# Kernel optimization log

Measured on AMD Instinct MI355X. Metric: run time of the kernel, lower is better.

Reference implementation:

```python
import jax, jax.numpy as jnp
import numpy as np

B, N, C_IN, C_OUT = 8, 4096, 64, 64
NEG_INF = -9e15
LEAKY_SLOPE = 0.01  # torch F.leaky_relu default


def setup_inputs() -> dict:
    key = jax.random.key(0)
    kx, ka, kw, kq, kk = jax.random.split(key, 5)
    X = jax.random.normal(kx, (B, N, C_IN), dtype=jnp.float32)
    A = jax.random.randint(ka, (N, N), 0, 2, dtype=jnp.int32)
    # xavier_uniform with gain=1.414 ~ scaled uniform; plain scaled normal is fine for a numeric reference
    def xavier(k, shape):
        fan_in, fan_out = shape
        bound = 1.414 * np.sqrt(6.0 / (fan_in + fan_out))
        return jax.random.uniform(k, shape, jnp.float32, -bound, bound)
    weight = xavier(kw, (C_IN, C_OUT))
    query = xavier(kq, (C_IN, C_OUT))
    key_p = xavier(kk, (C_IN, C_OUT))
    return {"X": X, "A": A, "weight": weight, "query": query, "key_p": key_p}


def reference(X, A, weight, query, key_p):
    n = X.shape[1]
    idx = jnp.arange(n)
    adj = A.at[idx, idx].set(1)  # add self-loops
    out = jnp.einsum('bni,io->bno', X, weight)
    q = jnp.einsum('bni,io->bno', X, query)
    k = jnp.einsum('bni,io->bno', X, key_p)
    att = jnp.einsum('bnd,bmd->bnm', q, k)          # QK^T, (B,N,N)
    att = jax.nn.leaky_relu(att, LEAKY_SLOPE)
    att = jnp.where(adj[None, :, :] > 0, att, NEG_INF)
    att = jax.nn.softmax(att, axis=-1)
    # dropout p=0 and/or eval mode -> identity
    return jnp.einsum('bnm,bmo->bno', att, out)
```

## Files before the change

### kernel.cpp

```cpp
#include <hip/hip_runtime.h>
#include <stdint.h>

#define BATCH 8
#define NN 4096
#define CC 64
#define MASKV -1.0e30f
#define LOG2E 1.4426950408889634f

typedef _Float16 half8 __attribute__((ext_vector_type(8)));
typedef __fp16 fp16x2 __attribute__((ext_vector_type(2)));
typedef float f32x4 __attribute__((ext_vector_type(4)));

__global__ __launch_bounds__(256) void gat_proj(
    const float* __restrict__ X, const float* __restrict__ W0,
    const float* __restrict__ Wq, const float* __restrict__ Wk,
    _Float16* __restrict__ qh, _Float16* __restrict__ ql,
    _Float16* __restrict__ kb, _Float16* __restrict__ vt)
{
    __shared__ alignas(16) _Float16 WTh[3][64][72];
    __shared__ alignas(16) _Float16 WTl[3][64][72];
    const int t = threadIdx.x;
    const float* Ws[3] = {W0, Wq, Wk};
    for (int e = t; e < 4096; e += 256) {
        int k = e >> 6, c = e & 63;
        #pragma unroll
        for (int m = 0; m < 3; ++m) {
            float w = Ws[m][e];
            _Float16 hi = (_Float16)w;
            WTh[m][c][k] = hi;
            WTl[m][c][k] = (_Float16)(w - (float)hi);
        }
    }
    __syncthreads();
    const int lane = t & 63, wv = t >> 6;
    const int cl = lane & 15, g = lane >> 4;
    {
        int tile = blockIdx.x * 4 + wv;
        int gr = tile * 16;
        const float* xr = X + (size_t)(gr + cl) * CC;
        half8 xh[2], xl[2];
        #pragma unroll
        for (int kf = 0; kf < 2; ++kf) {
            f32x4 a0 = *(const f32x4*)(xr + g*8 + kf*32);
            f32x4 a1 = *(const f32x4*)(xr + g*8 + kf*32 + 4);
            half8 h, l;
            #pragma unroll
            for (int j = 0; j < 4; ++j) {
                _Float16 h0 = (_Float16)a0[j], h1 = (_Float16)a1[j];
                h[j]   = h0; l[j]   = (_Float16)(a0[j] - (float)h0);
                h[j+4] = h1; l[j+4] = (_Float16)(a1[j] - (float)h1);
            }
            xh[kf] = h; xl[kf] = l;
        }
        #pragma unroll
        for (int mat = 1; mat <= 2; ++mat) {
            #pragma unroll
            for (int nt = 0; nt < 4; ++nt) {
                f32x4 acc = {0.f, 0.f, 0.f, 0.f};
                #pragma unroll
                for (int kf = 0; kf < 2; ++kf) {
                    half8 bh = *(const half8*)&WTh[mat][nt*16 + cl][g*8 + kf*32];
                    half8 bl = *(const half8*)&WTl[mat][nt*16 + cl][g*8 + kf*32];
                    acc = __builtin_amdgcn_mfma_f32_16x16x32_f16(xh[kf], bh, acc, 0, 0, 0);
                    acc = __builtin_amdgcn_mfma_f32_16x16x32_f16(xl[kf], bh, acc, 0, 0, 0);
                    acc = __builtin_amdgcn_mfma_f32_16x16x32_f16(xh[kf], bl, acc, 0, 0, 0);
                }
                #pragma unroll
                for (int i = 0; i < 4; ++i) {
                    size_t off = (size_t)(gr + 4*g + i) * CC + nt*16 + cl;
                    if (mat == 1) {
                        float qs = acc[i] * LOG2E;
                        _Float16 hi = (_Float16)qs;
                        qh[off] = hi;
                        ql[off] = (_Float16)(qs - (float)hi);
                    } else {
                        kb[off] = (_Float16)acc[i];
                    }
                }
            }
        }
        {
            int b = gr >> 12, n0 = gr & (NN - 1);
            #pragma unroll
            for (int mt = 0; mt < 4; ++mt) {
                f32x4 acc = {0.f, 0.f, 0.f, 0.f};
                #pragma unroll
                for (int kf = 0; kf < 2; ++kf) {
                    half8 ah = *(const half8*)&WTh[0][mt*16 + cl][g*8 + kf*32];
                    half8 al = *(const half8*)&WTl[0][mt*16 + cl][g*8 + kf*32];
                    acc = __builtin_amdgcn_mfma_f32_16x16x32_f16(ah, xh[kf], acc, 0, 0, 0);
                    acc = __builtin_amdgcn_mfma_f32_16x16x32_f16(al, xh[kf], acc, 0, 0, 0);
                    acc = __builtin_amdgcn_mfma_f32_16x16x32_f16(ah, xl[kf], acc, 0, 0, 0);
                }
                #pragma unroll
                for (int i = 0; i < 4; ++i) {
                    int co = mt*16 + 4*g + i;
                    vt[((size_t)b * CC + co) * NN + n0 + cl] = (_Float16)acc[i];
                }
            }
        }
    }
}

__global__ __launch_bounds__(256) void gat_mask(const int* __restrict__ A,
                                                unsigned short* __restrict__ M16)
{
    const int row = blockIdx.x;
    const int w16 = threadIdx.x;
    const int4* ap = (const int4*)(A + (size_t)row * NN + w16 * 16);
    unsigned m = 0;
    #pragma unroll
    for (int j = 0; j < 4; ++j) {
        int4 a = ap[j];
        m |= (a.x != 0 ? 1u : 0u) << (4*j);
        m |= (a.y != 0 ? 1u : 0u) << (4*j + 1);
        m |= (a.z != 0 ? 1u : 0u) << (4*j + 2);
        m |= (a.w != 0 ? 1u : 0u) << (4*j + 3);
    }
    if (w16 == (row >> 4)) m |= 1u << (row & 15);
    M16[(size_t)row * 256 + w16] = (unsigned short)m;
}

__global__ __launch_bounds__(256) void gat_attn(
    const _Float16* __restrict__ qh, const _Float16* __restrict__ ql,
    const _Float16* __restrict__ kf16, const _Float16* __restrict__ vtb,
    const unsigned long long* __restrict__ M,
    _Float16* __restrict__ po, float2* __restrict__ pml)
{
    __shared__ alignas(16) _Float16 Kt[64][72];
    __shared__ alignas(16) _Float16 Vt[64][72];
    __shared__ alignas(16) _Float16 Ps[4][32][72];
    const int t = threadIdx.x;
    const int lane = t & 63, wv = t >> 6;
    const int cl = lane & 15, g = lane >> 4;
    const int blk = blockIdx.x;
    const int b  = blk & 7;
    const int sp = (blk >> 3) & 3;
    const int qb = blk >> 5;
    const int Q0 = qb * 128 + wv * 32;
    const int c0 = sp * 16;

    half8 qfh[2][2], qfl[2][2];
    #pragma unroll
    for (int qt = 0; qt < 2; ++qt) {
        const _Float16* qrh = qh + ((size_t)b * NN + Q0 + qt*16 + cl) * CC;
        const _Float16* qrl = ql + ((size_t)b * NN + Q0 + qt*16 + cl) * CC;
        qfh[qt][0] = *(const half8*)(qrh + g*8);
        qfh[qt][1] = *(const half8*)(qrh + g*8 + 32);
        qfl[qt][0] = *(const half8*)(qrl + g*8);
        qfl[qt][1] = *(const half8*)(qrl + g*8 + 32);
    }
    const _Float16* kg = kf16 + (size_t)b * NN * CC;
    const _Float16* vg = vtb + (size_t)b * CC * NN;

    f32x4 o[2][4] = {};
    float m_run[2] = {MASKV, MASKV}, l_run[2] = {0.f, 0.f};

    uint4 pk0, pk1, pv0, pv1;
    unsigned long long pmA, pmB;
    auto loadchunk = [&](int kc) {
        const uint4* ks = (const uint4*)(kg + (size_t)kc * 64 * CC);
        pk0 = ks[t];
        pk1 = ks[t + 256];
        const _Float16* vs = vg + kc * 64;
        pv0 = *(const uint4*)(vs + (size_t)(t >> 3) * NN + (t & 7) * 8);
        pv1 = *(const uint4*)(vs + (size_t)((t >> 3) + 32) * NN + (t & 7) * 8);
        pmA = M[(size_t)(Q0 + cl) * 64 + kc];
        pmB = M[(size_t)(Q0 + 16 + cl) * 64 + kc];
    };
    loadchunk(c0);

    for (int kc = 0; kc < 16; ++kc) {
        __syncthreads();
        *(uint4*)&Kt[t >> 3][(t & 7) * 8] = pk0;
        *(uint4*)&Kt[(t >> 3) + 32][(t & 7) * 8] = pk1;
        *(uint4*)&Vt[t >> 3][(t & 7) * 8] = pv0;
        *(uint4*)&Vt[(t >> 3) + 32][(t & 7) * 8] = pv1;
        const unsigned long long cmA = pmA, cmB = pmB;
        __syncthreads();
        if (kc < 15) loadchunk(c0 + kc + 1);

        f32x4 sc[2][4] = {};
        #pragma unroll
        for (int kt = 0; kt < 4; ++kt) {
            #pragma unroll
            for (int kf = 0; kf < 2; ++kf) {
                half8 ka = *(const half8*)&Kt[kt*16 + cl][g*8 + kf*32];
                sc[0][kt] = __builtin_amdgcn_mfma_f32_16x16x32_f16(ka, qfh[0][kf], sc[0][kt], 0, 0, 0);
                sc[0][kt] = __builtin_amdgcn_mfma_f32_16x16x32_f16(ka, qfl[0][kf], sc[0][kt], 0, 0, 0);
                sc[1][kt] = __builtin_amdgcn_mfma_f32_16x16x32_f16(ka, qfh[1][kf], sc[1][kt], 0, 0, 0);
                sc[1][kt] = __builtin_amdgcn_mfma_f32_16x16x32_f16(ka, qfl[1][kf], sc[1][kt], 0, 0, 0);
            }
        }

        #pragma unroll
        for (int qt = 0; qt < 2; ++qt) {
            const unsigned long long cm = qt ? cmB : cmA;
            const unsigned mwx = (unsigned)cm, mwy = (unsigned)(cm >> 32);
            float sv[16];
            float mx = MASKV;
            #pragma unroll
            for (int kt = 0; kt < 4; ++kt) {
                unsigned wmw = (kt < 2) ? mwx : mwy;
                #pragma unroll
                for (int i = 0; i < 4; ++i) {
                    float x = sc[qt][kt][i];
                    x = fmaxf(x, 0.01f * x);
                    int bit = ((kt & 1) * 16) + 4*g + i;
                    x = ((wmw >> bit) & 1u) ? x : MASKV;
                    sv[kt*4 + i] = x;
                    mx = fmaxf(mx, x);
                }
            }
            mx = fmaxf(mx, __shfl_xor(mx, 16));
            mx = fmaxf(mx, __shfl_xor(mx, 32));
            if (__any(mx > m_run[qt])) {
                float nm = fmaxf(m_run[qt], mx);
                float alpha = __builtin_amdgcn_exp2f(m_run[qt] - nm);
                m_run[qt] = nm;
                l_run[qt] *= alpha;
                #pragma unroll
                for (int ct = 0; ct < 4; ++ct) o[qt][ct] *= alpha;
            }
            float lsum = 0.f;
            float p[16];
            #pragma unroll
            for (int j = 0; j < 16; ++j) {
                p[j] = __builtin_amdgcn_exp2f(sv[j] - m_run[qt]);
                lsum += p[j];
            }
            l_run[qt] += lsum;
            #pragma unroll
            for (int kt = 0; kt < 4; ++kt) {
                union { fp16x2 h; unsigned u; } p0u, p1u;
                p0u.h = __builtin_amdgcn_cvt_pkrtz(p[kt*4+0], p[kt*4+1]);
                p1u.h = __builtin_amdgcn_cvt_pkrtz(p[kt*4+2], p[kt*4+3]);
                uint2 pw = {p0u.u, p1u.u};
                *(uint2*)&Ps[wv][qt*16 + cl][kt*16 + 4*g] = pw;
            }
        }
        __builtin_amdgcn_wave_barrier();

        half8 pf[2][2];
        #pragma unroll
        for (int qt = 0; qt < 2; ++qt) {
            pf[qt][0] = *(const half8*)&Ps[wv][qt*16 + cl][g*8];
            pf[qt][1] = *(const half8*)&Ps[wv][qt*16 + cl][g*8 + 32];
        }
        #pragma unroll
        for (int ct = 0; ct < 4; ++ct) {
            half8 vf0 = *(const half8*)&Vt[ct*16 + cl][g*8];
            half8 vf1 = *(const half8*)&Vt[ct*16 + cl][g*8 + 32];
            #pragma unroll
            for (int qt = 0; qt < 2; ++qt) {
                o[qt][ct] = __builtin_amdgcn_mfma_f32_16x16x32_f16(vf0, pf[qt][0], o[qt][ct], 0, 0, 0);
                o[qt][ct] = __builtin_amdgcn_mfma_f32_16x16x32_f16(vf1, pf[qt][1], o[qt][ct], 0, 0, 0);
            }
        }
    }

    #pragma unroll
    for (int qt = 0; qt < 2; ++qt) {
        float lt = l_run[qt];
        lt += __shfl_xor(lt, 16);
        lt += __shfl_xor(lt, 32);
        size_t base = (size_t)sp * (BATCH * NN) + (size_t)b * NN + Q0 + qt*16 + cl;
        _Float16* orow = po + base * 64;
        #pragma unroll
        for (int ct = 0; ct < 4; ++ct) {
            union { fp16x2 h; unsigned u; } o0u, o1u;
            o0u.h = __builtin_amdgcn_cvt_pkrtz(o[qt][ct][0], o[qt][ct][1]);
            o1u.h = __builtin_amdgcn_cvt_pkrtz(o[qt][ct][2], o[qt][ct][3]);
            uint2 ow = {o0u.u, o1u.u};
            *(uint2*)(orow + ct*16 + 4*g) = ow;
        }
        if (g == 0) pml[base] = make_float2(m_run[qt], lt);
    }
}

__global__ __launch_bounds__(256) void gat_comb(
    const _Float16* __restrict__ po, const float2* __restrict__ pml,
    float* __restrict__ out)
{
    int gid = blockIdx.x * 256 + threadIdx.x;
    int row = gid >> 2;
    int col = (gid & 3) * 16;
    float2 ml[4];
    float Mx = MASKV;
    #pragma unroll
    for (int s = 0; s < 4; ++s) {
        ml[s] = pml[s * (BATCH * NN) + row];
        Mx = fmaxf(Mx, ml[s].x);
    }
    float w[4], den = 0.f;
    #pragma unroll
    for (int s = 0; s < 4; ++s) {
        w[s] = __builtin_amdgcn_exp2f(ml[s].x - Mx);
        den += w[s] * ml[s].y;
    }
    float inv = 1.0f / den;
    float acc[16] = {};
    #pragma unroll
    for (int s = 0; s < 4; ++s) {
        const _Float16* p = po + ((size_t)s * (BATCH * NN) + row) * 64 + col;
        float a = w[s] * inv;
        half8 v0 = *(const half8*)(p);
        half8 v1 = *(const half8*)(p + 8);
        #pragma unroll
        for (int j = 0; j < 8; ++j) {
            acc[j]     += a * (float)v0[j];
            acc[j + 8] += a * (float)v1[j];
        }
    }
    float* op = out + (size_t)row * 64 + col;
    #pragma unroll
    for (int i = 0; i < 4; ++i) {
        f32x4 r = {acc[4*i], acc[4*i+1], acc[4*i+2], acc[4*i+3]};
        *(f32x4*)(op + i*4) = r;
    }
}

extern "C" void kernel_launch(void* const* d_in, const int* in_sizes, int n_in,
                              void* d_out, int out_size, void* d_ws, size_t ws_size,
                              hipStream_t stream) {
    const float* X  = (const float*)d_in[0];
    const int*   A  = (const int*)d_in[1];
    const float* W0 = (const float*)d_in[2];
    const float* Wq = (const float*)d_in[3];
    const float* Wk = (const float*)d_in[4];
    float* out = (float*)d_out;
    char* ws = (char*)d_ws;
    const size_t SZ = (size_t)BATCH * NN * CC * 2;
    _Float16* qh  = (_Float16*)(ws);
    _Float16* ql  = (_Float16*)(ws + SZ);
    _Float16* kbf = (_Float16*)(ws + 2*SZ);
    _Float16* vtb = (_Float16*)(ws + 3*SZ);
    char* Mbase = ws + 4*SZ;
    _Float16* po = (_Float16*)(Mbase + 2*1024*1024);
    float2* pml  = (float2*)(Mbase + 2*1024*1024 + 4*SZ);

    hipLaunchKernelGGL(gat_proj, dim3(512),  dim3(256), 0, stream, X, W0, Wq, Wk, qh, ql, kbf, vtb);
    hipLaunchKernelGGL(gat_mask, dim3(4096), dim3(256), 0, stream, A, (unsigned short*)Mbase);
    hipLaunchKernelGGL(gat_attn, dim3(1024), dim3(256), 0, stream, qh, ql, kbf, vtb,
                       (const unsigned long long*)Mbase, po, pml);
    hipLaunchKernelGGL(gat_comb, dim3(512),  dim3(256), 0, stream, po, pml, out);
}
```

Before: 207.9 us.

## Use byte-mask adjacency, packed fp16 masking, XOR-swizzled LDS and MFMA priority

The mask kernel now writes a per-thread byte mask (16 MiB) laid out to match each lane's MFMA accumulator positions. The attention kernel applies the mask with packed fp16 bit operations and packed max, and zeroes masked probabilities by ANDing the mask. LDS tiles drop their padding in favour of an XOR swizzle. MFMA sections run at raised wave priority. The aim is fewer per-element shift/select ALU ops in the softmax and fewer LDS bank conflicts, at the cost of eight times more mask memory traffic and fp16 precision in the max and row-sum accumulation.

After: 209.6 us. Within noise of the previous version (+0.8%).

```diff
diff --git a/kernel.cpp b/kernel.cpp
--- a/kernel.cpp
+++ b/kernel.cpp
@@ -103,33 +103,35 @@
 }
 
 __global__ __launch_bounds__(256) void gat_mask(const int* __restrict__ A,
-                                                unsigned short* __restrict__ M16)
+                                                uint4* __restrict__ AM)
 {
-    const int row = blockIdx.x;
-    const int w16 = threadIdx.x;
-    const int4* ap = (const int4*)(A + (size_t)row * NN + w16 * 16);
-    unsigned m = 0;
-    #pragma unroll
-    for (int j = 0; j < 4; ++j) {
-        int4 a = ap[j];
-        m |= (a.x != 0 ? 1u : 0u) << (4*j);
-        m |= (a.y != 0 ? 1u : 0u) << (4*j + 1);
-        m |= (a.z != 0 ? 1u : 0u) << (4*j + 2);
-        m |= (a.w != 0 ? 1u : 0u) << (4*j + 3);
-    }
-    if (w16 == (row >> 4)) m |= 1u << (row & 15);
-    M16[(size_t)row * 256 + w16] = (unsigned short)m;
+    const int r = blockIdx.x;
+    const int t = threadIdx.x;
+    const int kc = t >> 2, g = t & 3;
+    unsigned w[4];
+    #pragma unroll
+    for (int kt = 0; kt < 4; ++kt) {
+        const int k0 = kc*64 + kt*16 + 4*g;
+        int4 a = *(const int4*)(A + (size_t)r * NN + k0);
+        unsigned m = 0;
+        m |= (a.x != 0 || k0     == r) ? 0x000000FFu : 0u;
+        m |= (a.y != 0 || k0 + 1 == r) ? 0x0000FF00u : 0u;
+        m |= (a.z != 0 || k0 + 2 == r) ? 0x00FF0000u : 0u;
+        m |= (a.w != 0 || k0 + 3 == r) ? 0xFF000000u : 0u;
+        w[kt] = m;
+    }
+    AM[(size_t)r * 256 + t] = make_uint4(w[0], w[1], w[2], w[3]);
 }
 
 __global__ __launch_bounds__(256) void gat_attn(
     const _Float16* __restrict__ qh, const _Float16* __restrict__ ql,
     const _Float16* __restrict__ kf16, const _Float16* __restrict__ vtb,
-    const unsigned long long* __restrict__ M,
+    const uint4* __restrict__ AM,
     _Float16* __restrict__ po, float2* __restrict__ pml)
 {
-    __shared__ alignas(16) _Float16 Kt[64][72];
-    __shared__ alignas(16) _Float16 Vt[64][72];
-    __shared__ alignas(16) _Float16 Ps[4][32][72];
+    __shared__ alignas(16) _Float16 Kt[64][64];
+    __shared__ alignas(16) _Float16 Vt[64][64];
+    __shared__ alignas(16) _Float16 Ps[4][32][64];
     const int t = threadIdx.x;
     const int lane = t & 63, wv = t >> 6;
     const int cl = lane & 15, g = lane >> 4;
@@ -139,6 +141,14 @@
     const int qb = blk >> 5;
     const int Q0 = qb * 128 + wv * 32;
     const int c0 = sp * 16;
+    const int swz = (cl & 7) << 4;
+
+    const int soff = (((t >> 3) * 128 + (t & 7) * 16) ^ (((t >> 3) & 7) << 4));
+    char* const kd0 = (char*)Kt + soff;
+    char* const kd1 = (char*)Kt + soff + 32 * 128;
+    char* const vd0 = (char*)Vt + soff;
+    char* const vd1 = (char*)Vt + soff + 32 * 128;
+    char* const psb = (char*)&Ps[wv][0][0];
 
     half8 qfh[2][2], qfl[2][2];
     #pragma unroll
@@ -156,8 +166,7 @@
     f32x4 o[2][4] = {};
     float m_run[2] = {MASKV, MASKV}, l_run[2] = {0.f, 0.f};
 
-    uint4 pk0, pk1, pv0, pv1;
-    unsigned long long pmA, pmB;
+    uint4 pk0, pk1, pv0, pv1, pa, pb;
     auto loadchunk = [&](int kc) {
         const uint4* ks = (const uint4*)(kg + (size_t)kc * 64 * CC);
         pk0 = ks[t];
@@ -165,53 +174,74 @@
         const _Float16* vs = vg + kc * 64;
         pv0 = *(const uint4*)(vs + (size_t)(t >> 3) * NN + (t & 7) * 8);
         pv1 = *(const uint4*)(vs + (size_t)((t >> 3) + 32) * NN + (t & 7) * 8);
-        pmA = M[(size_t)(Q0 + cl) * 64 + kc];
-        pmB = M[(size_t)(Q0 + 16 + cl) * 64 + kc];
+        pa = AM[(size_t)(Q0 + cl)      * 256 + kc * 4 + g];
+        pb = AM[(size_t)(Q0 + 16 + cl) * 256 + kc * 4 + g];
     };
     loadchunk(c0);
 
+    auto pkmax = [](unsigned a, unsigned b) {
+        unsigned d;
+        asm("v_pk_max_f16 %0, %1, %2" : "=v"(d) : "v"(a), "v"(b));
+        return d;
+    };
+
     for (int kc = 0; kc < 16; ++kc) {
         __syncthreads();
-        *(uint4*)&Kt[t >> 3][(t & 7) * 8] = pk0;
-        *(uint4*)&Kt[(t >> 3) + 32][(t & 7) * 8] = pk1;
-        *(uint4*)&Vt[t >> 3][(t & 7) * 8] = pv0;
-        *(uint4*)&Vt[(t >> 3) + 32][(t & 7) * 8] = pv1;
-        const unsigned long long cmA = pmA, cmB = pmB;
+        *(uint4*)kd0 = pk0;
+        *(uint4*)kd1 = pk1;
+        *(uint4*)vd0 = pv0;
+        *(uint4*)vd1 = pv1;
+        const uint4 ca = pa, cb = pb;
         __syncthreads();
         if (kc < 15) loadchunk(c0 + kc + 1);
 
+        __builtin_amdgcn_s_setprio(1);
         f32x4 sc[2][4] = {};
         #pragma unroll
         for (int kt = 0; kt < 4; ++kt) {
             #pragma unroll
             for (int kf = 0; kf < 2; ++kf) {
-                half8 ka = *(const half8*)&Kt[kt*16 + cl][g*8 + kf*32];
+                half8 ka = *(const half8*)((char*)Kt +
+                    ((((kt*16 + cl) * 128) + g*16 + kf*64) ^ swz));
                 sc[0][kt] = __builtin_amdgcn_mfma_f32_16x16x32_f16(ka, qfh[0][kf], sc[0][kt], 0, 0, 0);
                 sc[0][kt] = __builtin_amdgcn_mfma_f32_16x16x32_f16(ka, qfl[0][kf], sc[0][kt], 0, 0, 0);
                 sc[1][kt] = __builtin_amdgcn_mfma_f32_16x16x32_f16(ka, qfh[1][kf], sc[1][kt], 0, 0, 0);
                 sc[1][kt] = __builtin_amdgcn_mfma_f32_16x16x32_f16(ka, qfl[1][kf], sc[1][kt], 0, 0, 0);
             }
         }
+        __builtin_amdgcn_s_setprio(0);
 
         #pragma unroll
         for (int qt = 0; qt < 2; ++qt) {
-            const unsigned long long cm = qt ? cmB : cmA;
-            const unsigned mwx = (unsigned)cm, mwy = (unsigned)(cm >> 32);
+            const uint4 wm = qt ? cb : ca;
+            const unsigned am[4] = {wm.x, wm.y, wm.z, wm.w};
+            unsigned hm[8];
+            #pragma unroll
+            for (int kt = 0; kt < 4; ++kt) {
+                hm[2*kt]   = __builtin_amdgcn_perm(0u, am[kt], 0x01010000u);
+                hm[2*kt+1] = __builtin_amdgcn_perm(0u, am[kt], 0x03030202u);
+            }
             float sv[16];
-            float mx = MASKV;
+            #pragma unroll
+            for (int j = 0; j < 16; ++j) {
+                float x = sc[qt][j >> 2][j & 3];
+                sv[j] = fmaxf(x, 0.01f * x);
+            }
+            union UH { unsigned u; fp16x2 h; };
+            unsigned sm[8];
             #pragma unroll
             for (int kt = 0; kt < 4; ++kt) {
-                unsigned wmw = (kt < 2) ? mwx : mwy;
-                #pragma unroll
-                for (int i = 0; i < 4; ++i) {
-                    float x = sc[qt][kt][i];
-                    x = fmaxf(x, 0.01f * x);
-                    int bit = ((kt & 1) * 16) + 4*g + i;
-                    x = ((wmw >> bit) & 1u) ? x : MASKV;
-                    sv[kt*4 + i] = x;
-                    mx = fmaxf(mx, x);
-                }
-            }
+                UH s0, s1;
+                s0.h = __builtin_amdgcn_cvt_pkrtz(sv[4*kt + 0], sv[4*kt + 1]);
+                s1.h = __builtin_amdgcn_cvt_pkrtz(sv[4*kt + 2], sv[4*kt + 3]);
+                sm[2*kt]   = (hm[2*kt]   & s0.u) | (~hm[2*kt]   & 0xFC00FC00u);
+                sm[2*kt+1] = (hm[2*kt+1] & s1.u) | (~hm[2*kt+1] & 0xFC00FC00u);
+            }
+            unsigned tm = pkmax(
+                pkmax(pkmax(sm[0], sm[1]), pkmax(sm[2], sm[3])),
+                pkmax(pkmax(sm[4], sm[5]), pkmax(sm[6], sm[7])));
+            UH tmu; tmu.u = tm;
+            float mx = fmaxf((float)tmu.h[0], (float)tmu.h[1]);
             mx = fmaxf(mx, __shfl_xor(mx, 16));
             mx = fmaxf(mx, __shfl_xor(mx, 32));
             if (__any(mx > m_run[qt])) {
@@ -222,41 +252,45 @@
                 #pragma unroll
                 for (int ct = 0; ct < 4; ++ct) o[qt][ct] *= alpha;
             }
-            float lsum = 0.f;
             float p[16];
             #pragma unroll
-            for (int j = 0; j < 16; ++j) {
+            for (int j = 0; j < 16; ++j)
                 p[j] = __builtin_amdgcn_exp2f(sv[j] - m_run[qt]);
-                lsum += p[j];
-            }
-            l_run[qt] += lsum;
+            UH zz; zz.u = 0u;
+            fp16x2 acc2 = zz.h;
             #pragma unroll
             for (int kt = 0; kt < 4; ++kt) {
-                union { fp16x2 h; unsigned u; } p0u, p1u;
-                p0u.h = __builtin_amdgcn_cvt_pkrtz(p[kt*4+0], p[kt*4+1]);
-                p1u.h = __builtin_amdgcn_cvt_pkrtz(p[kt*4+2], p[kt*4+3]);
-                uint2 pw = {p0u.u, p1u.u};
-                *(uint2*)&Ps[wv][qt*16 + cl][kt*16 + 4*g] = pw;
-            }
+                UH w0, w1;
+                w0.h = __builtin_amdgcn_cvt_pkrtz(p[kt*4 + 0], p[kt*4 + 1]);
+                w1.h = __builtin_amdgcn_cvt_pkrtz(p[kt*4 + 2], p[kt*4 + 3]);
+                w0.u &= hm[2*kt];
+                w1.u &= hm[2*kt+1];
+                uint2 pw = {w0.u, w1.u};
+                *(uint2*)(psb + ((((qt*16 + cl) * 128) + kt*32 + g*8) ^ swz)) = pw;
+                acc2 += w0.h + w1.h;
+            }
+            l_run[qt] += (float)acc2[0] + (float)acc2[1];
         }
         __builtin_amdgcn_wave_barrier();
 
         half8 pf[2][2];
         #pragma unroll
         for (int qt = 0; qt < 2; ++qt) {
-            pf[qt][0] = *(const half8*)&Ps[wv][qt*16 + cl][g*8];
-            pf[qt][1] = *(const half8*)&Ps[wv][qt*16 + cl][g*8 + 32];
-        }
+            pf[qt][0] = *(const half8*)(psb + ((((qt*16 + cl) * 128) + g*16) ^ swz));
+            pf[qt][1] = *(const half8*)(psb + ((((qt*16 + cl) * 128) + g*16 + 64) ^ swz));
+        }
+        __builtin_amdgcn_s_setprio(1);
         #pragma unroll
         for (int ct = 0; ct < 4; ++ct) {
-            half8 vf0 = *(const half8*)&Vt[ct*16 + cl][g*8];
-            half8 vf1 = *(const half8*)&Vt[ct*16 + cl][g*8 + 32];
+            half8 vf0 = *(const half8*)((char*)Vt + ((((ct*16 + cl) * 128) + g*16) ^ swz));
+            half8 vf1 = *(const half8*)((char*)Vt + ((((ct*16 + cl) * 128) + g*16 + 64) ^ swz));
             #pragma unroll
             for (int qt = 0; qt < 2; ++qt) {
                 o[qt][ct] = __builtin_amdgcn_mfma_f32_16x16x32_f16(vf0, pf[qt][0], o[qt][ct], 0, 0, 0);
                 o[qt][ct] = __builtin_amdgcn_mfma_f32_16x16x32_f16(vf1, pf[qt][1], o[qt][ct], 0, 0, 0);
             }
         }
+        __builtin_amdgcn_s_setprio(0);
     }
 
     #pragma unroll
@@ -335,13 +369,13 @@
     _Float16* ql  = (_Float16*)(ws + SZ);
     _Float16* kbf = (_Float16*)(ws + 2*SZ);
     _Float16* vtb = (_Float16*)(ws + 3*SZ);
-    char* Mbase = ws + 4*SZ;
-    _Float16* po = (_Float16*)(Mbase + 2*1024*1024);
-    float2* pml  = (float2*)(Mbase + 2*1024*1024 + 4*SZ);
+    uint4* AMp    = (uint4*)(ws + 4*SZ);
+    _Float16* po  = (_Float16*)(ws + 4*SZ + (size_t)16*1024*1024);
+    float2* pml   = (float2*)(ws + 4*SZ + (size_t)32*1024*1024);
 
     hipLaunchKernelGGL(gat_proj, dim3(512),  dim3(256), 0, stream, X, W0, Wq, Wk, qh, ql, kbf, vtb);
-    hipLaunchKernelGGL(gat_mask, dim3(4096), dim3(256), 0, stream, A, (unsigned short*)Mbase);
+    hipLaunchKernelGGL(gat_mask, dim3(4096), dim3(256), 0, stream, A, AMp);
     hipLaunchKernelGGL(gat_attn, dim3(1024), dim3(256), 0, stream, qh, ql, kbf, vtb,
-                       (const unsigned long long*)Mbase, po, pml);
+                       AMp, po, pml);
     hipLaunchKernelGGL(gat_comb, dim3(512),  dim3(256), 0, stream, po, pml, out);
 }
```
